# Kernel optimization log

Hardware: AMD Instinct MI355X
Metric: run time of the kernel (lower is better)

Reference implementation:

```python
import jax, jax.numpy as jnp
import numpy as np

ALPHA = 0.2  # LeakyReLU negative slope
B, L, FIN, FOUT = 128, 512, 128, 128

def setup_inputs() -> dict:
    key = jax.random.key(0)
    k1, k2, k3, k4, k5 = jax.random.split(key, 5)
    h = jax.random.normal(k1, (B, L, FIN), jnp.float32)
    W = jax.random.normal(k2, (FIN, FOUT), jnp.float32) * (1.0 / np.sqrt(FIN))
    a = jax.random.normal(k3, (2 * FOUT,), jnp.float32) * (1.0 / np.sqrt(2 * FOUT))
    edge_bias = jax.random.normal(k4, (B, L, L), jnp.float32) * 0.1
    adj_mask = jax.random.uniform(k5, (L, L)) > 0.3
    adj_mask = adj_mask | jnp.eye(L, dtype=bool)  # self-loops avoid fully-masked rows
    return {"h": h, "W": W, "a": a, "edge_bias": edge_bias, "adj_mask": adj_mask}

def reference(h, W, a, edge_bias, adj_mask):
    # Wh: [B, L, Fout]
    Wh = jnp.einsum('blf,fo->blo', h, W)
    Fout = W.shape[1]
    # a([Wh_i, Wh_j]) == Wh_i @ a[:Fout] + Wh_j @ a[Fout:]  (avoids O(B*L*L*2F) concat)
    ei = Wh @ a[:Fout]   # [B, L]  (target i contribution)
    ej = Wh @ a[Fout:]   # [B, L]  (source j contribution)
    e = jax.nn.leaky_relu(ei[:, :, None] + ej[:, None, :], ALPHA) + edge_bias  # [B, L, L]
    e = jnp.where(adj_mask[None, :, :], e, -jnp.inf)
    att = jax.nn.softmax(e, axis=-1)  # dropout=0.0 -> identity
    h_prime = jnp.einsum('bij,bjo->bio', att, Wh)  # [B, L, Fout]
    return jax.nn.elu(h_prime)  # concat=True branch
```

## Files before the change

### kernel.cpp

```cpp
#include <hip/hip_runtime.h>
#include <string.h>

#define ALPHA 0.2f

typedef short short8 __attribute__((ext_vector_type(8)));
typedef float floatx4 __attribute__((ext_vector_type(4)));
typedef int intx4 __attribute__((ext_vector_type(4)));
typedef unsigned short ushort4v __attribute__((ext_vector_type(4)));

__device__ inline unsigned short f2bf(float f) {
    unsigned int v; __builtin_memcpy(&v, &f, 4);
    v = v + 0x7FFFu + ((v >> 16) & 1u);
    return (unsigned short)(v >> 16);
}

__device__ inline floatx4 ntload_f4(const float* p) {
    return __builtin_nontemporal_load((const floatx4*)p);
}

__global__ __launch_bounds__(512, 4) void wh_kernel(const float* __restrict__ h,
                                                    const float* __restrict__ W,
                                                    const float* __restrict__ a,
                                                    unsigned short* __restrict__ wht,
                                                    float* __restrict__ ei,
                                                    float* __restrict__ ej)
{
    __shared__ __align__(16) unsigned short h_s[128][136];
    __shared__ __align__(16) unsigned short w_s[128][136];
    __shared__ float a_s[256];
    const int tid  = threadIdx.x;
    const int lane = tid & 63;
    const int wv   = tid >> 6;
    const int quad = lane >> 4;
    const int l16  = lane & 15;
    const int r0   = blockIdx.x * 128;
    const int b    = r0 >> 9;
    const int jb   = r0 & 511;

    const float* hbase = h + (size_t)r0 * 128;
#pragma unroll
    for (int it = 0; it < 8; ++it) {
        int idx4 = it * 512 + tid;
        floatx4 v = ntload_f4(hbase + idx4 * 4);
        int row = idx4 >> 5;
        int col = (idx4 & 31) * 4;
        ushort4v u;
        for (int e = 0; e < 4; ++e) u[e] = f2bf(v[e]);
        *(ushort4v*)&h_s[row][col] = u;
    }
#pragma unroll
    for (int it = 0; it < 32; ++it) {
        int idx = it * 512 + tid;
        w_s[idx & 127][idx >> 7] = f2bf(W[idx]);
    }
    if (tid < 256) a_s[tid] = a[tid];
    __syncthreads();

    floatx4 acc[8];
#pragma unroll
    for (int mo = 0; mo < 8; ++mo) acc[mo] = (floatx4)0.f;

#pragma unroll
    for (int kk = 0; kk < 4; ++kk) {
        short8 bfr = *(const short8*)&h_s[wv * 16 + l16][kk * 32 + quad * 8];
#pragma unroll
        for (int mo = 0; mo < 8; ++mo) {
            short8 afr = *(const short8*)&w_s[mo * 16 + l16][kk * 32 + quad * 8];
            acc[mo] = __builtin_amdgcn_mfma_f32_16x16x32_bf16(afr, bfr, acc[mo], 0, 0, 0);
        }
    }

    {
        float si = 0.f, sj = 0.f;
#pragma unroll
        for (int mo = 0; mo < 8; ++mo)
            for (int r = 0; r < 4; ++r) {
                int o = mo * 16 + quad * 4 + r;
                float v = acc[mo][r];
                si += v * a_s[o];
                sj += v * a_s[128 + o];
            }
        si += __shfl_xor(si, 16); si += __shfl_xor(si, 32);
        sj += __shfl_xor(sj, 16); sj += __shfl_xor(sj, 32);
        if (quad == 0) {
            int j = jb + wv * 16 + l16;
            ei[b * 512 + j] = si;
            ej[b * 512 + j] = sj;
        }
    }

#pragma unroll
    for (int mo = 0; mo < 8; ++mo)
        for (int r = 0; r < 4; ++r) {
            int o = mo * 16 + quad * 4 + r;
            int j = jb + wv * 16 + l16;
            wht[(size_t)b * 65536 + o * 512 + j] = f2bf(acc[mo][r]);
        }
}

__global__ __launch_bounds__(512, 8) void attn_kernel(const unsigned short* __restrict__ wht,
                                                      const float* __restrict__ ei,
                                                      const float* __restrict__ ej,
                                                      const float* __restrict__ bias,
                                                      const int* __restrict__ adj,
                                                      float* __restrict__ out)
{
    __shared__ __align__(16) unsigned short p_s[32][520];
    __shared__ float ei_s[32];
    __shared__ float s_row[32];

    const int tid  = threadIdx.x;
    const int lane = tid & 63;
    const int wv   = tid >> 6;
    const int quad = lane >> 4;
    const int l16  = lane & 15;
    const int b    = blockIdx.x >> 4;
    const int i0   = (blockIdx.x & 15) * 32;

    const float* bp = bias + ((size_t)(b * 512 + i0 + wv * 4)) * 512;
    const int*   ap = adj + (i0 + wv * 4) * 512;
    floatx4 bb0 = ntload_f4(bp + lane * 4);
    floatx4 bb1 = ntload_f4(bp + 256 + lane * 4);
    intx4   mm0 = *(const intx4*)(ap + lane * 4);
    intx4   mm1 = *(const intx4*)(ap + 256 + lane * 4);

    const floatx4 ejv0 = *(const floatx4*)(ej + b * 512 + lane * 4);
    const floatx4 ejv1 = *(const floatx4*)(ej + b * 512 + 256 + lane * 4);
    if (tid < 32) ei_s[tid] = ei[b * 512 + i0 + tid];
    __syncthreads();

    float rsum[4];

#pragma unroll
    for (int rr = 0; rr < 4; ++rr) {
        floatx4 nb0, nb1; intx4 nm0, nm1;
        if (rr < 3) {
            nb0 = ntload_f4(bp + 512 + lane * 4);
            nb1 = ntload_f4(bp + 768 + lane * 4);
            nm0 = *(const intx4*)(ap + 512 + lane * 4);
            nm1 = *(const intx4*)(ap + 768 + lane * 4);
        }
        const int il = wv * 4 + rr;
        const float eiv = ei_s[il];
        float sm = 0.f;
        ushort4v p0, p1;
        for (int e = 0; e < 4; ++e) {
            float x = eiv + ejv0[e];
            x = fmaxf(x, ALPHA * x);
            x += bb0[e];
            float p = __expf(x);
            p = (mm0[e] != 0) ? p : 0.f;
            sm += p;
            p0[e] = f2bf(p);
        }
        for (int e = 0; e < 4; ++e) {
            float x = eiv + ejv1[e];
            x = fmaxf(x, ALPHA * x);
            x += bb1[e];
            float p = __expf(x);
            p = (mm1[e] != 0) ? p : 0.f;
            sm += p;
            p1[e] = f2bf(p);
        }
        *(ushort4v*)&p_s[il][lane * 4]       = p0;
        *(ushort4v*)&p_s[il][256 + lane * 4] = p1;
        rsum[rr] = sm;
        bb0 = nb0; bb1 = nb1; mm0 = nm0; mm1 = nm1;
        bp += 512; ap += 512;
    }

    const unsigned short* wb = wht + (size_t)b * 65536 + (wv * 16 + l16) * 512 + quad * 8;
    short8 bf = *(const short8*)(wb);

#pragma unroll
    for (int rr = 0; rr < 4; ++rr)
        for (int off = 32; off; off >>= 1)
            rsum[rr] += __shfl_xor(rsum[rr], off);
    if (lane == 0)
#pragma unroll
        for (int rr = 0; rr < 4; ++rr) s_row[wv * 4 + rr] = rsum[rr];
    __syncthreads();

    floatx4 acc[2];
    acc[0] = (floatx4)0.f;
    acc[1] = (floatx4)0.f;

#pragma unroll
    for (int k16 = 0; k16 < 16; ++k16) {
        int ko = k16 * 32 + quad * 8;
        short8 nbf;
        if (k16 < 15) nbf = *(const short8*)(wb + (k16 + 1) * 32);
        short8 af0 = *(const short8*)&p_s[l16][ko];
        short8 af1 = *(const short8*)&p_s[16 + l16][ko];
        acc[0] = __builtin_amdgcn_mfma_f32_16x16x32_bf16(af0, bf, acc[0], 0, 0, 0);
        acc[1] = __builtin_amdgcn_mfma_f32_16x16x32_bf16(af1, bf, acc[1], 0, 0, 0);
        bf = nbf;
    }

#pragma unroll
    for (int m = 0; m < 2; ++m)
        for (int r = 0; r < 4; ++r) {
            int il = m * 16 + quad * 4 + r;
            int o  = wv * 16 + l16;
            float v = acc[m][r] / s_row[il];
            v = v > 0.f ? v : (__expf(v) - 1.f);
            __builtin_nontemporal_store(v, &out[((size_t)(b * 512 + i0 + il)) * 128 + o]);
        }
}

extern "C" void kernel_launch(void* const* d_in, const int* in_sizes, int n_in,
                              void* d_out, int out_size, void* d_ws, size_t ws_size,
                              hipStream_t stream)
{
    const float* h    = (const float*)d_in[0];
    const float* W    = (const float*)d_in[1];
    const float* a    = (const float*)d_in[2];
    const float* bias = (const float*)d_in[3];
    const int*   adj  = (const int*)d_in[4];
    float*       out  = (float*)d_out;

    unsigned short* wht = (unsigned short*)d_ws;
    float* ei = (float*)((char*)d_ws + 16777216);
    float* ej = ei + 65536;

    hipLaunchKernelGGL(wh_kernel,   dim3(512),  dim3(512), 0, stream, h, W, a, wht, ei, ej);
    hipLaunchKernelGGL(attn_kernel, dim3(2048), dim3(512), 0, stream, wht, ei, ej, bias, adj, out);
}
```

Baseline: 264.7 us.

## Build attention fragments in registers and feed MFMA directly, skipping LDS staging

The attention kernel is restructured so each wave owns 16 query rows and computes the masked exponentials straight into MFMA A-fragment registers, accumulating all 128 output features per wave. This removes the shared-memory probability tile and the extra barrier that went with it. Bias and mask are now streamed per 32-column tile with register prefetch, and Wh fragments are read directly from global memory for each tile. The trade-off is more accumulator registers, smaller 256-thread blocks, and more global traffic for Wh fragments, which are reloaded by every wave and block.

```diff
diff --git a/kernel.cpp b/kernel.cpp
--- a/kernel.cpp
+++ b/kernel.cpp
@@ -98,113 +98,118 @@
         }
 }
 
-__global__ __launch_bounds__(512, 8) void attn_kernel(const unsigned short* __restrict__ wht,
-                                                      const float* __restrict__ ei,
-                                                      const float* __restrict__ ej,
-                                                      const float* __restrict__ bias,
-                                                      const int* __restrict__ adj,
-                                                      float* __restrict__ out)
+__global__ __launch_bounds__(256, 4) void attn_fused(const unsigned short* __restrict__ wht,
+                                                     const float* __restrict__ ei,
+                                                     const float* __restrict__ ej,
+                                                     const float* __restrict__ bias,
+                                                     const int* __restrict__ adj,
+                                                     float* __restrict__ out)
 {
-    __shared__ __align__(16) unsigned short p_s[32][520];
-    __shared__ float ei_s[32];
-    __shared__ float s_row[32];
+    __shared__ __align__(16) float ej_s[512];
+    __shared__ float s_row_s[64];
 
     const int tid  = threadIdx.x;
     const int lane = tid & 63;
     const int wv   = tid >> 6;
     const int quad = lane >> 4;
     const int l16  = lane & 15;
-    const int b    = blockIdx.x >> 4;
-    const int i0   = (blockIdx.x & 15) * 32;
-
-    const float* bp = bias + ((size_t)(b * 512 + i0 + wv * 4)) * 512;
-    const int*   ap = adj + (i0 + wv * 4) * 512;
-    floatx4 bb0 = ntload_f4(bp + lane * 4);
-    floatx4 bb1 = ntload_f4(bp + 256 + lane * 4);
-    intx4   mm0 = *(const intx4*)(ap + lane * 4);
-    intx4   mm1 = *(const intx4*)(ap + 256 + lane * 4);
-
-    const floatx4 ejv0 = *(const floatx4*)(ej + b * 512 + lane * 4);
-    const floatx4 ejv1 = *(const floatx4*)(ej + b * 512 + 256 + lane * 4);
-    if (tid < 32) ei_s[tid] = ei[b * 512 + i0 + tid];
+    const int b    = blockIdx.x >> 3;
+    const int i0   = (blockIdx.x & 7) * 64;
+    const int iw   = i0 + wv * 16;
+
+    const float* bp = bias + ((size_t)(b * 512 + iw + l16)) * 512 + quad * 8;
+    const int*   ap = adj + (iw + l16) * 512 + quad * 8;
+    const unsigned short* wbase = wht + (size_t)b * 65536 + l16 * 512 + quad * 8;
+
+    floatx4 cb0 = ntload_f4(bp);
+    floatx4 cb1 = ntload_f4(bp + 4);
+    intx4   cm0 = *(const intx4*)(ap);
+    intx4   cm1 = *(const intx4*)(ap + 4);
+    const float eiv = ei[b * 512 + iw + l16];
+
+    if (tid < 128) *(floatx4*)&ej_s[tid * 4] = *(const floatx4*)(ej + b * 512 + tid * 4);
     __syncthreads();
 
-    float rsum[4];
-
-#pragma unroll
-    for (int rr = 0; rr < 4; ++rr) {
+    floatx4 acc[8];
+#pragma unroll
+    for (int mo = 0; mo < 8; ++mo) acc[mo] = (floatx4)0.f;
+
+    float rsum = 0.f;
+
+#pragma unroll
+    for (int jt = 0; jt < 16; ++jt) {
+        short8 wfa[4];
+#pragma unroll
+        for (int mo = 0; mo < 4; ++mo)
+            wfa[mo] = *(const short8*)(wbase + mo * 16 * 512 + jt * 32);
+
         floatx4 nb0, nb1; intx4 nm0, nm1;
-        if (rr < 3) {
-            nb0 = ntload_f4(bp + 512 + lane * 4);
-            nb1 = ntload_f4(bp + 768 + lane * 4);
-            nm0 = *(const intx4*)(ap + 512 + lane * 4);
-            nm1 = *(const intx4*)(ap + 768 + lane * 4);
-        }
-        const int il = wv * 4 + rr;
-        const float eiv = ei_s[il];
+        if (jt < 15) {
+            nb0 = ntload_f4(bp + (jt + 1) * 32);
+            nb1 = ntload_f4(bp + (jt + 1) * 32 + 4);
+            nm0 = *(const intx4*)(ap + (jt + 1) * 32);
+            nm1 = *(const intx4*)(ap + (jt + 1) * 32 + 4);
+        }
+
+        floatx4 ejv0 = *(const floatx4*)&ej_s[jt * 32 + quad * 8];
+        floatx4 ejv1 = *(const floatx4*)&ej_s[jt * 32 + quad * 8 + 4];
+
+        short8 af;
         float sm = 0.f;
-        ushort4v p0, p1;
+#pragma unroll
         for (int e = 0; e < 4; ++e) {
             float x = eiv + ejv0[e];
             x = fmaxf(x, ALPHA * x);
-            x += bb0[e];
+            x += cb0[e];
             float p = __expf(x);
-            p = (mm0[e] != 0) ? p : 0.f;
+            p = (cm0[e] != 0) ? p : 0.f;
             sm += p;
-            p0[e] = f2bf(p);
-        }
+            af[e] = (short)f2bf(p);
+        }
+#pragma unroll
         for (int e = 0; e < 4; ++e) {
             float x = eiv + ejv1[e];
             x = fmaxf(x, ALPHA * x);
-            x += bb1[e];
+            x += cb1[e];
             float p = __expf(x);
-            p = (mm1[e] != 0) ? p : 0.f;
+            p = (cm1[e] != 0) ? p : 0.f;
             sm += p;
-            p1[e] = f2bf(p);
-        }
-        *(ushort4v*)&p_s[il][lane * 4]       = p0;
-        *(ushort4v*)&p_s[il][256 + lane * 4] = p1;
-        rsum[rr] = sm;
-        bb0 = nb0; bb1 = nb1; mm0 = nm0; mm1 = nm1;
-        bp += 512; ap += 512;
-    }
-
-    const unsigned short* wb = wht + (size_t)b * 65536 + (wv * 16 + l16) * 512 + quad * 8;
-    short8 bf = *(const short8*)(wb);
-
-#pragma unroll
-    for (int rr = 0; rr < 4; ++rr)
-        for (int off = 32; off; off >>= 1)
-            rsum[rr] += __shfl_xor(rsum[rr], off);
-    if (lane == 0)
-#pragma unroll
-        for (int rr = 0; rr < 4; ++rr) s_row[wv * 4 + rr] = rsum[rr];
+            af[4 + e] = (short)f2bf(p);
+        }
+        rsum += sm;
+
+        short8 wfb[4];
+#pragma unroll
+        for (int mo = 0; mo < 4; ++mo)
+            wfb[mo] = *(const short8*)(wbase + (mo + 4) * 16 * 512 + jt * 32);
+
+#pragma unroll
+        for (int mo = 0; mo < 4; ++mo)
+            acc[mo] = __builtin_amdgcn_mfma_f32_16x16x32_bf16(af, wfa[mo], acc[mo], 0, 0, 0);
+#pragma unroll
+        for (int mo = 0; mo < 4; ++mo)
+            acc[mo + 4] = __builtin_amdgcn_mfma_f32_16x16x32_bf16(af, wfb[mo], acc[mo + 4], 0, 0, 0);
+
+        cb0 = nb0; cb1 = nb1; cm0 = nm0; cm1 = nm1;
+    }
+
+    rsum += __shfl_xor(rsum, 16);
+    rsum += __shfl_xor(rsum, 32);
+    if (lane < 16) s_row_s[wv * 16 + lane] = rsum;
     __syncthreads();
 
-    floatx4 acc[2];
-    acc[0] = (floatx4)0.f;
-    acc[1] = (floatx4)0.f;
-
-#pragma unroll
-    for (int k16 = 0; k16 < 16; ++k16) {
-        int ko = k16 * 32 + quad * 8;
-        short8 nbf;
-        if (k16 < 15) nbf = *(const short8*)(wb + (k16 + 1) * 32);
-        short8 af0 = *(const short8*)&p_s[l16][ko];
-        short8 af1 = *(const short8*)&p_s[16 + l16][ko];
-        acc[0] = __builtin_amdgcn_mfma_f32_16x16x32_bf16(af0, bf, acc[0], 0, 0, 0);
-        acc[1] = __builtin_amdgcn_mfma_f32_16x16x32_bf16(af1, bf, acc[1], 0, 0, 0);
-        bf = nbf;
-    }
-
-#pragma unroll
-    for (int m = 0; m < 2; ++m)
+    float inv[4];
+#pragma unroll
+    for (int r = 0; r < 4; ++r) inv[r] = 1.0f / s_row_s[wv * 16 + quad * 4 + r];
+
+#pragma unroll
+    for (int mo = 0; mo < 8; ++mo)
+#pragma unroll
         for (int r = 0; r < 4; ++r) {
-            int il = m * 16 + quad * 4 + r;
-            int o  = wv * 16 + l16;
-            float v = acc[m][r] / s_row[il];
+            int i = iw + quad * 4 + r;
+            float v = acc[mo][r] * inv[r];
             v = v > 0.f ? v : (__expf(v) - 1.f);
-            __builtin_nontemporal_store(v, &out[((size_t)(b * 512 + i0 + il)) * 128 + o]);
+            out[((size_t)(b * 512 + i)) * 128 + mo * 16 + l16] = v;
         }
 }
 
@@ -224,5 +229,5 @@
     float* ej = ei + 65536;
 
     hipLaunchKernelGGL(wh_kernel,   dim3(512),  dim3(512), 0, stream, h, W, a, wht, ei, ej);
-    hipLaunchKernelGGL(attn_kernel, dim3(2048), dim3(512), 0, stream, wht, ei, ej, bias, adj, out);
-}
+    hipLaunchKernelGGL(attn_fused,  dim3(1024), dim3(256), 0, stream, wht, ei, ej, bias, adj, out);
+}
```

After: 294.9 us. 1.11x slower.
